# Kernel tuning notes

Hardware: AMD Instinct MI355X
Metric: run time of the kernel (lower is better)

Reference implementation:

```python
import jax, jax.numpy as jnp
import numpy as np

G, N, F_IN = 1024, 256, 128
HID = [256, 256, 256]
KS = [32, 16, 8]
N_OUT = 2


def _graph_conv(adj, x, W, b, act):
    # DGL GraphConv, norm='both': h = D^{-1/2} A D^{-1/2} X W + b
    deg = adj.sum(-1)                                   # [G, n]
    norm = jax.lax.rsqrt(jnp.maximum(deg, 1.0))[..., None]
    h = (x * norm) @ W                                  # [G, n, d_out]
    h = jnp.einsum('gnm,gmd->gnd', adj, h) * norm + b
    return act(h) if act is not None else h


def _sag_pool(adj, x, Ws, bs, k):
    # SAGPool: score via GraphConv, keep top-k nodes, gate by tanh(score),
    # take induced subgraph adjacency.
    score = _graph_conv(adj, x, Ws, bs, None)[..., 0]   # [G, n]
    sv, idx = jax.lax.top_k(score, k)                   # [G, k]
    x_sel = jnp.take_along_axis(x, idx[:, :, None], axis=1) * jnp.tanh(sv)[:, :, None]
    a = jnp.take_along_axis(adj, idx[:, :, None], axis=1)
    a = jnp.take_along_axis(a, idx[:, None, :], axis=2)  # [G, k, k]
    return a, x_sel


def _sum_max_readout(x):
    return jnp.concatenate([x.sum(axis=1), x.max(axis=1)], axis=-1)  # [G, 2d]


def setup_inputs() -> dict:
    key = jax.random.key(0)
    ks = jax.random.split(key, 16)
    feat = jax.random.normal(ks[0], (G, N, F_IN), dtype=jnp.float32)
    # sparse-ish symmetric binary adjacency, avg degree ~ 16
    a = (jax.random.uniform(ks[1], (G, N, N)) < (16.0 / N)).astype(jnp.float32)
    adj = jnp.maximum(a, jnp.swapaxes(a, 1, 2))

    def glorot(k, shp):
        lim = float(np.sqrt(6.0 / (shp[0] + shp[1])))
        return jax.random.uniform(k, shp, jnp.float32, -lim, lim)

    dims = [F_IN] + HID
    inp = {'feat': feat, 'adj': adj}
    for i in range(3):
        inp[f'W{i}'] = glorot(ks[2 + i], (dims[i], dims[i + 1]))
        inp[f'b{i}'] = jnp.zeros((dims[i + 1],), jnp.float32)
        inp[f'Ws{i}'] = glorot(ks[5 + i], (dims[i + 1], 1))
        inp[f'bs{i}'] = jnp.zeros((1,), jnp.float32)
    inp['Wd1'] = glorot(ks[8], (2 * sum(HID), 128))
    inp['bd1'] = jnp.zeros((128,), jnp.float32)
    inp['Wd2'] = glorot(ks[9], (128, N_OUT))
    inp['bd2'] = jnp.zeros((N_OUT,), jnp.float32)
    return inp


def reference(feat, adj, W0, b0, Ws0, bs0, W1, b1, Ws1, bs1, W2, b2, Ws2, bs2,
              Wd1, bd1, Wd2, bd2):
    act = jax.nn.leaky_relu  # F.leaky_relu, slope 0.01
    Wgs = [(W0, b0), (W1, b1), (W2, b2)]
    Wss = [(Ws0, bs0), (Ws1, bs1), (Ws2, bs2)]
    readouts = []
    x, a = feat, adj
    for i in range(3):
        x = _graph_conv(a, x, Wgs[i][0], Wgs[i][1], act)
        a, x = _sag_pool(a, x, Wss[i][0], Wss[i][1], KS[i])
        readouts.append(_sum_max_readout(x))
    merged = jnp.concatenate(readouts, axis=1)          # [G, 2*sum(HID)]
    # dropout omitted (deterministic eval reference)
    h = act(merged @ Wd1 + bd1)
    out = jax.nn.sigmoid(h @ Wd2 + bd2)                 # [G, n_output]
    return out
```

## Files before the change

### kernel.cpp

```cpp
#include <hip/hip_runtime.h>
#include <math.h>

constexpr int GG  = 1024;
constexpr int NN  = 256;
constexpr int FF  = 128;
constexpr int DD  = 256;
constexpr int KS0 = 32, KS1 = 16, KS2 = 8;

__device__ __forceinline__ float lrelu(float x){ return x >= 0.f ? x : 0.01f*x; }

__device__ __forceinline__ unsigned short f2bf(float f) {
  unsigned u = __float_as_uint(f);
  unsigned r = (u + 0x7FFFu + ((u >> 16) & 1u)) >> 16;
  return (unsigned short)r;
}
__device__ __forceinline__ float bf2f(unsigned short h) {
  return __uint_as_float(((unsigned)h) << 16);
}

typedef __attribute__((ext_vector_type(8)))  __bf16 bf16x8;
typedef __attribute__((ext_vector_type(16))) float  f32x16;

union Frag8 { unsigned short us[8]; unsigned long long u64[2]; bf16x8 v; };

typedef __attribute__((address_space(1))) void gvoid;
typedef __attribute__((address_space(3))) void lvoid;
__device__ __forceinline__ void async_cp16(const unsigned short* g, unsigned short* l) {
  __builtin_amdgcn_global_load_lds((const gvoid*)g, (lvoid*)l, 16, 0, 0);
}

__global__ void k_splitW_all(const float* __restrict__ Wa, const float* __restrict__ Wb,
                             const float* __restrict__ Wc,
                             unsigned short* __restrict__ oa, unsigned short* __restrict__ ob,
                             unsigned short* __restrict__ oc) {
  int e = blockIdx.x*256 + threadIdx.x;
  if (e >= FF*DD + 2*DD*DD) return;
  const float* W; unsigned short* out; int K;
  if (e < FF*DD)                { W = Wa; out = oa; K = FF; }
  else if (e < FF*DD + DD*DD)   { e -= FF*DD; W = Wb; out = ob; K = DD; }
  else                          { e -= FF*DD + DD*DD; W = Wc; out = oc; K = DD; }
  int j    = e & 7;
  int lane = (e >> 3) & 63;
  int nt   = (e >> 9) & 7;
  int s    = (e >> 12) & 1;
  int kti  = e >> 13;
  int n = nt*32 + (lane & 31);
  int k = kti*32 + s*16 + ((lane >> 5) << 3) + j;
  float x = W[(size_t)k*DD + n];
  unsigned short h1 = f2bf(x);  float r1 = x - bf2f(h1);
  unsigned short h2 = f2bf(r1); float r2 = r1 - bf2f(h2);
  unsigned short h3 = f2bf(r2);
  out[e] = h1; out[DD*K + e] = h2; out[2*DD*K + e] = h3;
}

__global__ void k_maskrow(const float* __restrict__ adj, float* __restrict__ norm0,
                          unsigned long long* __restrict__ mask) {
  int row = blockIdx.x*4 + (threadIdx.x >> 6);
  int lane = threadIdx.x & 63;
  const float* ar = adj + (size_t)row*NN;
  float f0 = ar[lane], f1 = ar[64 + lane], f2 = ar[128 + lane], f3 = ar[192 + lane];
  unsigned long long m0 = __ballot(f0 > 0.5f);
  unsigned long long m1 = __ballot(f1 > 0.5f);
  unsigned long long m2 = __ballot(f2 > 0.5f);
  unsigned long long m3 = __ballot(f3 > 0.5f);
  if (lane < 4) {
    unsigned long long mm = lane == 0 ? m0 : lane == 1 ? m1 : lane == 2 ? m2 : m3;
    mask[(size_t)row*4 + lane] = mm;
  }
  if (lane == 0) {
    int cnt = __popcll(m0) + __popcll(m1) + __popcll(m2) + __popcll(m3);
    norm0[row] = rsqrtf(fmaxf((float)cnt, 1.0f));
  }
}

__global__ __launch_bounds__(256, 4) void k_spmm_s(
    const float* __restrict__ feat, const unsigned long long* __restrict__ mask,
    const float* __restrict__ norm0, float* __restrict__ T0) {
  constexpr int ST = 36;
  __shared__ float ls[NN*ST];
  __shared__ float snorm[NN];
  int bid = blockIdx.x;
  int g = bid >> 2, q = bid & 3;
  int t = threadIdx.x;
  const float* Xg = feat + (size_t)g*NN*FF + q*32;

  snorm[t] = norm0[g*NN + t];
  const unsigned long long* mp = mask + ((size_t)g*NN + t)*4;
  unsigned long long mrow[4];
  #pragma unroll
  for (int w = 0; w < 4; ++w) mrow[w] = mp[w];
  __syncthreads();

  #pragma unroll
  for (int i = 0; i < 8; ++i) {
    int e = t + i*256;
    int r = e >> 3, c4 = (e & 7)*4;
    float4 v = *reinterpret_cast<const float4*>(Xg + (size_t)r*FF + c4);
    float nv = snorm[r];
    v.x *= nv; v.y *= nv; v.z *= nv; v.w *= nv;
    *reinterpret_cast<float4*>(&ls[r*ST + c4]) = v;
  }
  __syncthreads();

  float4 acc[8];
  #pragma unroll
  for (int i = 0; i < 8; ++i) acc[i] = make_float4(0.f, 0.f, 0.f, 0.f);
  #pragma unroll
  for (int w = 0; w < 4; ++w) {
    unsigned long long m = mrow[w];
    while (m) {
      int c = __builtin_ctzll(m);
      const float4* xp = reinterpret_cast<const float4*>(&ls[(w*64 + c)*ST]);
      #pragma unroll
      for (int i = 0; i < 8; ++i) {
        float4 v = xp[i];
        acc[i].x += v.x; acc[i].y += v.y; acc[i].z += v.z; acc[i].w += v.w;
      }
      m &= m - 1;
    }
  }
  float* op = T0 + ((size_t)g*NN + t)*FF + q*32;
  #pragma unroll
  for (int i = 0; i < 8; ++i)
    *reinterpret_cast<float4*>(op + i*4) = acc[i];
}

__global__ __launch_bounds__(256, 2) void k_gemm0(
    const float* __restrict__ Tmat, const unsigned short* __restrict__ Wk,
    const float* __restrict__ normv, const float* __restrict__ bias,
    const float* __restrict__ Ws, float* __restrict__ hs) {
  __shared__ unsigned short bsh[3*8192];
  int t = threadIdx.x;
  int lane = t & 63, wave = t >> 6;
  int lm = lane & 31, lh = lane >> 5;
  int rowbase = blockIdx.x*128 + wave*32;

  f32x16 acc[8];
  #pragma unroll
  for (int nt = 0; nt < 8; ++nt) acc[nt] = (f32x16)0.0f;

  for (int kti = 0; kti < 4; ++kti) {
    int kt = kti*32;
    float4 af[2][2];
    #pragma unroll
    for (int s = 0; s < 2; ++s) {
      const float* ap = Tmat + (size_t)(rowbase + lm)*FF + kt + s*16 + lh*8;
      af[s][0] = *reinterpret_cast<const float4*>(ap);
      af[s][1] = *reinterpret_cast<const float4*>(ap + 4);
    }
    __syncthreads();
    #pragma unroll
    for (int sp = 0; sp < 3; ++sp)
      #pragma unroll
      for (int r = 0; r < 4; ++r) {
        const unsigned short* src = Wk + (size_t)sp*DD*FF + (size_t)kti*8192 + r*2048 + t*8;
        unsigned short* dst = bsh + sp*8192 + r*2048 + t*8;
        async_cp16(src, dst);
      }
    __syncthreads();
    Frag8 afr[2][3];
    #pragma unroll
    for (int s = 0; s < 2; ++s) {
      const float* fv = &af[s][0].x;
      #pragma unroll
      for (int j = 0; j < 8; ++j) {
        float x = fv[j];
        unsigned short h1 = f2bf(x);  float r1 = x - bf2f(h1);
        unsigned short h2 = f2bf(r1); float r2 = r1 - bf2f(h2);
        afr[s][0].us[j] = h1; afr[s][1].us[j] = h2; afr[s][2].us[j] = f2bf(r2);
      }
    }
    #pragma unroll
    for (int s = 0; s < 2; ++s)
      #pragma unroll
      for (int nt = 0; nt < 8; ++nt) {
        const unsigned short* bp = bsh + ((s*8 + nt)*64 + lane)*8;
        Frag8 b0_, b1_, b2_;
        b0_.v = *reinterpret_cast<const bf16x8*>(bp);
        b1_.v = *reinterpret_cast<const bf16x8*>(bp + 8192);
        b2_.v = *reinterpret_cast<const bf16x8*>(bp + 16384);
        acc[nt] = __builtin_amdgcn_mfma_f32_32x32x16_bf16(afr[s][0].v, b0_.v, acc[nt], 0,0,0);
        acc[nt] = __builtin_amdgcn_mfma_f32_32x32x16_bf16(afr[s][0].v, b1_.v, acc[nt], 0,0,0);
        acc[nt] = __builtin_amdgcn_mfma_f32_32x32x16_bf16(afr[s][1].v, b0_.v, acc[nt], 0,0,0);
        acc[nt] = __builtin_amdgcn_mfma_f32_32x32x16_bf16(afr[s][0].v, b2_.v, acc[nt], 0,0,0);
        acc[nt] = __builtin_amdgcn_mfma_f32_32x32x16_bf16(afr[s][2].v, b0_.v, acc[nt], 0,0,0);
        acc[nt] = __builtin_amdgcn_mfma_f32_32x32x16_bf16(afr[s][1].v, b1_.v, acc[nt], 0,0,0);
      }
  }

  float bcol[8], wcol[8];
  #pragma unroll
  for (int nt = 0; nt < 8; ++nt) { int col = nt*32 + lm; bcol[nt] = bias[col]; wcol[nt] = Ws[col]; }
  float hsum[16];
  #pragma unroll
  for (int r = 0; r < 16; ++r) {
    int row = rowbase + (r & 3) + 8*(r >> 2) + 4*lh;
    float nv = normv[row];
    float hp = 0.f;
    #pragma unroll
    for (int nt = 0; nt < 8; ++nt) hp += lrelu(nv*acc[nt][r] + bcol[nt])*wcol[nt];
    hsum[r] = hp;
  }
  #pragma unroll
  for (int off = 1; off <= 16; off <<= 1)
    #pragma unroll
    for (int r = 0; r < 16; ++r) hsum[r] += __shfl_xor(hsum[r], off);
  if (lm == 0)
    #pragma unroll
    for (int r = 0; r < 16; ++r) {
      int row = rowbase + (r & 3) + 8*(r >> 2) + 4*lh;
      hs[row] = normv[row]*hsum[r];
    }
}

__global__ __launch_bounds__(256) void k_topk_sel0(
    const unsigned long long* __restrict__ mask, const float* __restrict__ hs,
    const float* __restrict__ norm0, const float* __restrict__ bs,
    const float* __restrict__ T0, const float* __restrict__ W0,
    const float* __restrict__ b0, float* __restrict__ x_sel,
    float* __restrict__ a1, float* __restrict__ merged) {
  __shared__ float sh[NN];
  __shared__ float ssc[NN];
  __shared__ float sT[KS0*FF];
  __shared__ int sidx[KS0]; __shared__ float stv[KS0]; __shared__ float snv[KS0];
  int g = blockIdx.x, t = threadIdx.x;

  sh[t] = hs[g*NN + t];
  __syncthreads();
  const unsigned long long* mr = mask + ((size_t)g*NN + t)*4;
  float s = 0.f;
  #pragma unroll
  for (int w = 0; w < 4; ++w) {
    unsigned long long m = mr[w];
    const float* base = sh + w*64;
    while (m) {
      int c = __builtin_ctzll(m);
      s += base[c];
      m &= m - 1;
    }
  }
  ssc[t] = norm0[g*NN + t]*s + bs[0];
  __syncthreads();
  if (t < 64) {
    float sv[4]; int si[4];
    #pragma unroll
    for (int e = 0; e < 4; ++e) { sv[e] = ssc[e*64 + t]; si[e] = e*64 + t; }
    for (int kk = 0; kk < KS0; ++kk) {
      float bs_ = -INFINITY; int bi = 1 << 30;
      #pragma unroll
      for (int e = 0; e < 4; ++e)
        if (sv[e] > bs_ || (sv[e] == bs_ && si[e] < bi)) { bs_ = sv[e]; bi = si[e]; }
      for (int off = 32; off; off >>= 1) {
        float os = __shfl_xor(bs_, off);
        int oi = __shfl_xor(bi, off);
        if (os > bs_ || (os == bs_ && oi < bi)) { bs_ = os; bi = oi; }
      }
      if (t == 0) { sidx[kk] = bi; stv[kk] = tanhf(bs_); }
      #pragma unroll
      for (int e = 0; e < 4; ++e) if (si[e] == bi) sv[e] = -INFINITY;
    }
  }
  __syncthreads();
  if (t < KS0) snv[t] = norm0[g*NN + sidx[t]];
  #pragma unroll
  for (int i = 0; i < 4; ++i) {
    int e4 = t + i*256;
    int r = e4 >> 5, c4 = e4 & 31;
    reinterpret_cast<float4*>(sT)[e4] =
        *reinterpret_cast<const float4*>(&T0[((size_t)g*NN + sidx[r])*FF + c4*4]);
  }
  __syncthreads();
  float sum[KS0];
  #pragma unroll
  for (int j = 0; j < KS0; ++j) sum[j] = 0.f;
  for (int k = 0; k < FF; k += 4) {
    float4 w;
    w.x = W0[(size_t)(k+0)*DD + t]; w.y = W0[(size_t)(k+1)*DD + t];
    w.z = W0[(size_t)(k+2)*DD + t]; w.w = W0[(size_t)(k+3)*DD + t];
    #pragma unroll
    for (int j = 0; j < KS0; ++j) {
      float4 tv4 = *reinterpret_cast<const float4*>(&sT[j*FF + k]);
      sum[j] += tv4.x*w.x + tv4.y*w.y + tv4.z*w.z + tv4.w*w.w;
    }
  }
  float b = b0[t];
  float ssum = 0.f, mx = -INFINITY;
  #pragma unroll
  for (int j = 0; j < KS0; ++j) {
    float val = lrelu(snv[j]*sum[j] + b) * stv[j];
    x_sel[((size_t)g*KS0 + j)*DD + t] = val;
    ssum += val; mx = fmaxf(mx, val);
  }
  merged[(size_t)g*1536 + t] = ssum;
  merged[(size_t)g*1536 + 256 + t] = mx;
  for (int e = t; e < KS0*KS0; e += 256) {
    int r = e >> 5, c = e & 31;
    int nr = sidx[r], nc = sidx[c];
    unsigned long long m = mask[((size_t)g*NN + nr)*4 + (nc >> 6)];
    a1[(size_t)g*KS0*KS0 + e] = (float)((m >> (nc & 63)) & 1ull);
  }
}

__global__ __launch_bounds__(256, 2) void k_fused1(
    const float* __restrict__ a, const float* __restrict__ xin,
    const unsigned short* __restrict__ Wk, const float* __restrict__ bias,
    const float* __restrict__ Ws, const float* __restrict__ bs,
    float* __restrict__ x_sel_out, float* __restrict__ a_out,
    float* __restrict__ merged) {
  constexpr int n = KS0;
  constexpr int kp = KS1;
  constexpr int TP = DD + 4;
  __shared__ float sa[n*n];
  __shared__ float bufA[n*DD];
  __shared__ float sT[n*TP];
  __shared__ float snorm[n]; __shared__ float shs[n]; __shared__ float ssc[n];
  __shared__ int sidx[kp]; __shared__ float stv[kp];
  int g = blockIdx.x, t = threadIdx.x;
  int lane = t & 63, wave = t >> 6, lm = lane & 31, lh = lane >> 5;

  for (int e = t; e < n*n; e += 256) sa[e] = a[(size_t)g*n*n + e];
  __syncthreads();
  if (t < n) {
    float dg = 0.f;
    for (int m = 0; m < n; ++m) dg += sa[m*n + t];
    snorm[t] = rsqrtf(fmaxf(dg, 1.f));
  }
  __syncthreads();
  {
    const float4* xp = reinterpret_cast<const float4*>(xin + (size_t)g*n*DD);
    #pragma unroll
    for (int i = 0; i < (n*DD/4)/256; ++i) {
      int e4 = t + i*256;
      float4 v = xp[e4];
      float nv = snorm[e4 >> 6];
      v.x *= nv; v.y *= nv; v.z *= nv; v.w *= nv;
      reinterpret_cast<float4*>(bufA)[e4] = v;
    }
  }
  __syncthreads();
  {
    float acc2[n];
    #pragma unroll
    for (int r = 0; r < n; ++r) acc2[r] = 0.f;
    for (int m = 0; m < n; ++m) {
      float xv = bufA[m*DD + t];
      #pragma unroll
      for (int r = 0; r < n; ++r) acc2[r] += sa[r*n + m]*xv;
    }
    #pragma unroll
    for (int r = 0; r < n; ++r) sT[r*TP + t] = acc2[r];
  }
  __syncthreads();

  f32x16 acc[2];
  acc[0] = (f32x16)0.0f; acc[1] = (f32x16)0.0f;
  for (int kti = 0; kti < DD/32; ++kti) {
    int kt = kti*32;
    Frag8 afr[2][3];
    #pragma unroll
    for (int s = 0; s < 2; ++s) {
      float4 af4[2];
      const float* ap = &sT[lm*TP + kt + s*16 + lh*8];
      af4[0] = *reinterpret_cast<const float4*>(ap);
      af4[1] = *reinterpret_cast<const float4*>(ap + 4);
      const float* fv = &af4[0].x;
      #pragma unroll
      for (int j = 0; j < 8; ++j) {
        float x = fv[j];
        unsigned short h1 = f2bf(x);  float r1 = x - bf2f(h1);
        unsigned short h2 = f2bf(r1); float r2 = r1 - bf2f(h2);
        afr[s][0].us[j] = h1; afr[s][1].us[j] = h2; afr[s][2].us[j] = f2bf(r2);
      }
    }
    #pragma unroll
    for (int s = 0; s < 2; ++s)
      #pragma unroll
      for (int ntl = 0; ntl < 2; ++ntl) {
        int ct = wave*2 + ntl;
        size_t boff = ((((size_t)kti*2 + s)*8 + ct)*64 + lane)*8;
        Frag8 b0_, b1_, b2_;
        b0_.v = *reinterpret_cast<const bf16x8*>(Wk + boff);
        b1_.v = *reinterpret_cast<const bf16x8*>(Wk + (size_t)DD*DD + boff);
        b2_.v = *reinterpret_cast<const bf16x8*>(Wk + (size_t)2*DD*DD + boff);
        acc[ntl] = __builtin_amdgcn_mfma_f32_32x32x16_bf16(afr[s][0].v, b0_.v, acc[ntl], 0,0,0);
        acc[ntl] = __builtin_amdgcn_mfma_f32_32x32x16_bf16(afr[s][0].v, b1_.v, acc[ntl], 0,0,0);
        acc[ntl] = __builtin_amdgcn_mfma_f32_32x32x16_bf16(afr[s][1].v, b0_.v, acc[ntl], 0,0,0);
        acc[ntl] = __builtin_amdgcn_mfma_f32_32x32x16_bf16(afr[s][0].v, b2_.v, acc[ntl], 0,0,0);
        acc[ntl] = __builtin_amdgcn_mfma_f32_32x32x16_bf16(afr[s][2].v, b0_.v, acc[ntl], 0,0,0);
        acc[ntl] = __builtin_amdgcn_mfma_f32_32x32x16_bf16(afr[s][1].v, b1_.v, acc[ntl], 0,0,0);
      }
  }

  #pragma unroll
  for (int ntl = 0; ntl < 2; ++ntl) {
    int colbase = wave*64 + ntl*32 + lm;
    float bc = bias[colbase];
    #pragma unroll
    for (int r = 0; r < 16; ++r) {
      int row = (r & 3) + 8*(r >> 2) + 4*lh;
      bufA[row*DD + colbase] = lrelu(snorm[row]*acc[ntl][r] + bc);
    }
  }
  __syncthreads();
  if (wave == 0) {
    float wcol[8];
    #pragma unroll
    for (int nt = 0; nt < 8; ++nt) wcol[nt] = Ws[nt*32 + lm];
    float hsum[16];
    #pragma unroll
    for (int r = 0; r < 16; ++r) {
      int row = (r & 3) + 8*(r >> 2) + 4*lh;
      float hp = 0.f;
      #pragma unroll
      for (int nt = 0; nt < 8; ++nt) hp += bufA[row*DD + nt*32 + lm]*wcol[nt];
      hsum[r] = hp;
    }
    #pragma unroll
    for (int off = 1; off <= 16; off <<= 1)
      #pragma unroll
      for (int r = 0; r < 16; ++r) hsum[r] += __shfl_xor(hsum[r], off);
    if (lm == 0)
      #pragma unroll
      for (int r = 0; r < 16; ++r) {
        int row = (r & 3) + 8*(r >> 2) + 4*lh;
        shs[row] = snorm[row]*hsum[r];
      }
  }
  __syncthreads();
  if (t < n) {
    float s = 0.f;
    for (int m = 0; m < n; ++m) s += sa[m*n + t]*shs[m];
    ssc[t] = snorm[t]*s + bs[0];
  }
  __syncthreads();
  if (t < 64) {
    float sc = (t < n) ? ssc[t] : -INFINITY;
    int si = (t < n) ? t : (1 << 30);
    for (int kk = 0; kk < kp; ++kk) {
      float bs_ = sc; int bi = si;
      for (int off = 32; off; off >>= 1) {
        float os = __shfl_xor(bs_, off);
        int oi = __shfl_xor(bi, off);
        if (os > bs_ || (os == bs_ && oi < bi)) { bs_ = os; bi = oi; }
      }
      if (t == 0) { sidx[kk] = bi; stv[kk] = tanhf(bs_); }
      if (si == bi) sc = -INFINITY;
    }
  }
  __syncthreads();
  float sum = 0.f, mx = -INFINITY;
  #pragma unroll
  for (int j = 0; j < kp; ++j) {
    float v = bufA[sidx[j]*DD + t] * stv[j];
    x_sel_out[((size_t)g*kp + j)*DD + t] = v;
    sum += v; mx = fmaxf(mx, v);
  }
  merged[(size_t)g*1536 + 512 + t] = sum;
  merged[(size_t)g*1536 + 768 + t] = mx;
  { int r = t >> 4, c = t & 15;
    a_out[(size_t)g*kp*kp + t] = sa[sidx[r]*n + sidx[c]]; }
}

__global__ __launch_bounds__(256, 2) void k_fused2(
    const float* __restrict__ a, const float* __restrict__ xin,
    const unsigned short* __restrict__ Wk, const float* __restrict__ bias,
    const float* __restrict__ Ws, const float* __restrict__ bs,
    float* __restrict__ merged) {
  constexpr int n = KS1;
  constexpr int kp = KS2;
  constexpr int TP = DD + 4;
  __shared__ float sa[n*n];
  __shared__ float bufA[n*DD];
  __shared__ float sT[n*TP];
  __shared__ float snorm[n]; __shared__ float shs[n]; __shared__ float ssc[n];
  __shared__ int sidx[kp]; __shared__ float stv[kp];
  int g = blockIdx.x, t = threadIdx.x;
  int lane = t & 63, wave = t >> 6, lm = lane & 31, lh = lane >> 5;

  for (int e = t; e < n*n; e += 256) sa[e] = a[(size_t)g*n*n + e];
  __syncthreads();
  if (t < n) {
    float dg = 0.f;
    for (int m = 0; m < n; ++m) dg += sa[m*n + t];
    snorm[t] = rsqrtf(fmaxf(dg, 1.f));
  }
  __syncthreads();
  {
    const float4* xp = reinterpret_cast<const float4*>(xin + (size_t)g*n*DD);
    #pragma unroll
    for (int i = 0; i < (n*DD/4)/256; ++i) {
      int e4 = t + i*256;
      float4 v = xp[e4];
      float nv = snorm[e4 >> 6];
      v.x *= nv; v.y *= nv; v.z *= nv; v.w *= nv;
      reinterpret_cast<float4*>(bufA)[e4] = v;
    }
  }
  __syncthreads();
  {
    float acc2[n];
    #pragma unroll
    for (int r = 0; r < n; ++r) acc2[r] = 0.f;
    for (int m = 0; m < n; ++m) {
      float xv = bufA[m*DD + t];
      #pragma unroll
      for (int r = 0; r < n; ++r) acc2[r] += sa[r*n + m]*xv;
    }
    #pragma unroll
    for (int r = 0; r < n; ++r) sT[r*TP + t] = acc2[r];
  }
  __syncthreads();

  f32x16 acc[2];
  acc[0] = (f32x16)0.0f; acc[1] = (f32x16)0.0f;
  for (int kti = 0; kti < DD/32; ++kti) {
    int kt = kti*32;
    Frag8 afr[2][3];
    #pragma unroll
    for (int s = 0; s < 2; ++s) {
      float4 af4[2];
      if (lm < n) {
        const float* ap = &sT[lm*TP + kt + s*16 + lh*8];
        af4[0] = *reinterpret_cast<const float4*>(ap);
        af4[1] = *reinterpret_cast<const float4*>(ap + 4);
      } else {
        af4[0] = make_float4(0.f, 0.f, 0.f, 0.f);
        af4[1] = make_float4(0.f, 0.f, 0.f, 0.f);
      }
      const float* fv = &af4[0].x;
      #pragma unroll
      for (int j = 0; j < 8; ++j) {
        float x = fv[j];
        unsigned short h1 = f2bf(x);  float r1 = x - bf2f(h1);
        unsigned short h2 = f2bf(r1); float r2 = r1 - bf2f(h2);
        afr[s][0].us[j] = h1; afr[s][1].us[j] = h2; afr[s][2].us[j] = f2bf(r2);
      }
    }
    #pragma unroll
    for (int s = 0; s < 2; ++s)
      #pragma unroll
      for (int ntl = 0; ntl < 2; ++ntl) {
        int ct = wave*2 + ntl;
        size_t boff = ((((size_t)kti*2 + s)*8 + ct)*64 + lane)*8;
        Frag8 b0_, b1_, b2_;
        b0_.v = *reinterpret_cast<const bf16x8*>(Wk + boff);
        b1_.v = *reinterpret_cast<const bf16x8*>(Wk + (size_t)DD*DD + boff);
        b2_.v = *reinterpret_cast<const bf16x8*>(Wk + (size_t)2*DD*DD + boff);
        acc[ntl] = __builtin_amdgcn_mfma_f32_32x32x16_bf16(afr[s][0].v, b0_.v, acc[ntl], 0,0,0);
        acc[ntl] = __builtin_amdgcn_mfma_f32_32x32x16_bf16(afr[s][0].v, b1_.v, acc[ntl], 0,0,0);
        acc[ntl] = __builtin_amdgcn_mfma_f32_32x32x16_bf16(afr[s][1].v, b0_.v, acc[ntl], 0,0,0);
        acc[ntl] = __builtin_amdgcn_mfma_f32_32x32x16_bf16(afr[s][0].v, b2_.v, acc[ntl], 0,0,0);
        acc[ntl] = __builtin_amdgcn_mfma_f32_32x32x16_bf16(afr[s][2].v, b0_.v, acc[ntl], 0,0,0);
        acc[ntl] = __builtin_amdgcn_mfma_f32_32x32x16_bf16(afr[s][1].v, b1_.v, acc[ntl], 0,0,0);
      }
  }

  #pragma unroll
  for (int ntl = 0; ntl < 2; ++ntl) {
    int colbase = wave*64 + ntl*32 + lm;
    float bc = bias[colbase];
    #pragma unroll
    for (int r = 0; r < 16; ++r) {
      int row = (r & 3) + 8*(r >> 2) + 4*lh;
      if (row < n) bufA[row*DD + colbase] = lrelu(snorm[row]*acc[ntl][r] + bc);
    }
  }
  __syncthreads();
  if (wave == 0) {
    float wcol[8];
    #pragma unroll
    for (int nt = 0; nt < 8; ++nt) wcol[nt] = Ws[nt*32 + lm];
    float hsum[16];
    #pragma unroll
    for (int r = 0; r < 16; ++r) {
      int row = (r & 3) + 8*(r >> 2) + 4*lh;
      float hp = 0.f;
      if (row < n) {
        #pragma unroll
        for (int nt = 0; nt < 8; ++nt) hp += bufA[row*DD + nt*32 + lm]*wcol[nt];
      }
      hsum[r] = hp;
    }
    #pragma unroll
    for (int off = 1; off <= 16; off <<= 1)
      #pragma unroll
      for (int r = 0; r < 16; ++r) hsum[r] += __shfl_xor(hsum[r], off);
    if (lm == 0)
      #pragma unroll
      for (int r = 0; r < 16; ++r) {
        int row = (r & 3) + 8*(r >> 2) + 4*lh;
        if (row < n) shs[row] = snorm[row]*hsum[r];
      }
  }
  __syncthreads();
  if (t < n) {
    float s = 0.f;
    for (int m = 0; m < n; ++m) s += sa[m*n + t]*shs[m];
    ssc[t] = snorm[t]*s + bs[0];
  }
  __syncthreads();
  if (t < 64) {
    float sc = (t < n) ? ssc[t] : -INFINITY;
    int si = (t < n) ? t : (1 << 30);
    for (int kk = 0; kk < kp; ++kk) {
      float bs_ = sc; int bi = si;
      for (int off = 32; off; off >>= 1) {
        float os = __shfl_xor(bs_, off);
        int oi = __shfl_xor(bi, off);
        if (os > bs_ || (os == bs_ && oi < bi)) { bs_ = os; bi = oi; }
      }
      if (t == 0) { sidx[kk] = bi; stv[kk] = tanhf(bs_); }
      if (si == bi) sc = -INFINITY;
    }
  }
  __syncthreads();
  float sum = 0.f, mx = -INFINITY;
  #pragma unroll
  for (int j = 0; j < kp; ++j) {
    float v = bufA[sidx[j]*DD + t] * stv[j];
    sum += v; mx = fmaxf(mx, v);
  }
  merged[(size_t)g*1536 + 1024 + t] = sum;
  merged[(size_t)g*1536 + 1280 + t] = mx;
}

__global__ void k_mlp(const float* __restrict__ merged, const float* __restrict__ Wd1,
                      const float* __restrict__ bd1, const float* __restrict__ Wd2,
                      const float* __restrict__ bd2, float* __restrict__ out) {
  __shared__ float sm[4*1536];
  __shared__ float sh[4][128];
  int g0 = blockIdx.x*4; int t = threadIdx.x;
  for (int i = t; i < 4*1536; i += 128) sm[i] = merged[(size_t)g0*1536 + i];
  __syncthreads();
  float a0 = 0.f, a1 = 0.f, a2 = 0.f, a3 = 0.f;
  for (int kk = 0; kk < 1536; ++kk) {
    float w = Wd1[(size_t)kk*128 + t];
    a0 += sm[kk]*w; a1 += sm[1536 + kk]*w; a2 += sm[3072 + kk]*w; a3 += sm[4608 + kk]*w;
  }
  float b = bd1[t];
  sh[0][t] = lrelu(a0 + b); sh[1][t] = lrelu(a1 + b);
  sh[2][t] = lrelu(a2 + b); sh[3][t] = lrelu(a3 + b);
  __syncthreads();
  if (t < 8) {
    int gi = t >> 1, c = t & 1;
    float o = 0.f;
    for (int kk = 0; kk < 128; ++kk) o += sh[gi][kk]*Wd2[kk*2 + c];
    out[(size_t)(g0 + gi)*2 + c] = 1.f/(1.f + expf(-(o + bd2[c])));
  }
}

extern "C" void kernel_launch(void* const* d_in, const int* in_sizes, int n_in,
                              void* d_out, int out_size, void* d_ws, size_t ws_size,
                              hipStream_t stream) {
  const float* feat = (const float*)d_in[0];
  const float* adj  = (const float*)d_in[1];
  const float* W0 = (const float*)d_in[2];  const float* b0  = (const float*)d_in[3];
  const float* Ws0= (const float*)d_in[4];  const float* bs0 = (const float*)d_in[5];
  const float* W1 = (const float*)d_in[6];  const float* b1  = (const float*)d_in[7];
  const float* Ws1= (const float*)d_in[8];  const float* bs1 = (const float*)d_in[9];
  const float* W2 = (const float*)d_in[10]; const float* b2  = (const float*)d_in[11];
  const float* Ws2= (const float*)d_in[12]; const float* bs2 = (const float*)d_in[13];
  const float* Wd1= (const float*)d_in[14]; const float* bd1 = (const float*)d_in[15];
  const float* Wd2= (const float*)d_in[16]; const float* bd2 = (const float*)d_in[17];
  float* out = (float*)d_out;

  char* ws = (char*)d_ws;
  size_t off = 0;
  auto alloc = [&](size_t bytes) -> char* {
    char* p = ws + off; off += (bytes + 255) & ~(size_t)255; return p;
  };
  float* norm0 = (float*)alloc((size_t)GG*NN*4);
  unsigned long long* mask0 = (unsigned long long*)alloc((size_t)GG*NN*4*8);
  float* hs0   = (float*)alloc((size_t)GG*NN*4);
  float* merged= (float*)alloc((size_t)GG*1536*4);
  unsigned short* W0s = (unsigned short*)alloc((size_t)3*FF*DD*2);
  unsigned short* W1s = (unsigned short*)alloc((size_t)3*DD*DD*2);
  unsigned short* W2s = (unsigned short*)alloc((size_t)3*DD*DD*2);
  float* T0     = (float*)alloc((size_t)GG*NN*FF*4);
  float* x_sel1 = (float*)alloc((size_t)GG*KS0*DD*4);
  float* a1     = (float*)alloc((size_t)GG*KS0*KS0*4);
  float* x_sel2 = (float*)alloc((size_t)GG*KS1*DD*4);
  float* a2     = (float*)alloc((size_t)GG*KS1*KS1*4);

  k_splitW_all<<<(FF*DD + 2*DD*DD)/256, 256, 0, stream>>>(W0, W1, W2, W0s, W1s, W2s);

  k_maskrow<<<GG*NN/4, 256, 0, stream>>>(adj, norm0, mask0);
  k_spmm_s<<<4*GG, 256, 0, stream>>>(feat, mask0, norm0, T0);
  k_gemm0<<<GG*NN/128, 256, 0, stream>>>(T0, W0s, norm0, b0, Ws0, hs0);
  k_topk_sel0<<<GG, 256, 0, stream>>>(mask0, hs0, norm0, bs0, T0, W0, b0, x_sel1, a1, merged);

  k_fused1<<<GG, 256, 0, stream>>>(a1, x_sel1, W1s, b1, Ws1, bs1, x_sel2, a2, merged);

  k_fused2<<<GG, 256, 0, stream>>>(a2, x_sel2, W2s, b2, Ws2, bs2, merged);

  k_mlp<<<GG/4, 128, 0, stream>>>(merged, Wd1, bd1, Wd2, bd2, out);

  (void)in_sizes; (void)n_in; (void)out_size; (void)ws_size;
}
```

Before: 915.5 us.

## Fuse layer-0 GEMM score computation with top-k selection into one per-graph kernel

```diff
diff --git a/kernel.cpp b/kernel.cpp
--- a/kernel.cpp
+++ b/kernel.cpp
@@ -125,15 +125,23 @@
     *reinterpret_cast<float4*>(op + i*4) = acc[i];
 }
 
-__global__ __launch_bounds__(256, 2) void k_gemm0(
+__global__ __launch_bounds__(512, 2) void k_gemm_topk0(
     const float* __restrict__ Tmat, const unsigned short* __restrict__ Wk,
     const float* __restrict__ normv, const float* __restrict__ bias,
-    const float* __restrict__ Ws, float* __restrict__ hs) {
+    const float* __restrict__ Ws, const unsigned long long* __restrict__ mask,
+    const float* __restrict__ bs, const float* __restrict__ W0,
+    const float* __restrict__ b0, float* __restrict__ x_sel,
+    float* __restrict__ a1, float* __restrict__ merged) {
   __shared__ unsigned short bsh[3*8192];
+  __shared__ float shs[NN];
+  __shared__ float ssc[NN];
+  __shared__ int sidx[KS0]; __shared__ float stv[KS0]; __shared__ float snv[KS0];
+  int g = blockIdx.x;
   int t = threadIdx.x;
   int lane = t & 63, wave = t >> 6;
   int lm = lane & 31, lh = lane >> 5;
-  int rowbase = blockIdx.x*128 + wave*32;
+  int rowbase = wave*32;
+  const size_t growbase = (size_t)g*NN;
 
   f32x16 acc[8];
   #pragma unroll
@@ -144,19 +152,18 @@
     float4 af[2][2];
     #pragma unroll
     for (int s = 0; s < 2; ++s) {
-      const float* ap = Tmat + (size_t)(rowbase + lm)*FF + kt + s*16 + lh*8;
+      const float* ap = Tmat + (growbase + rowbase + lm)*FF + kt + s*16 + lh*8;
       af[s][0] = *reinterpret_cast<const float4*>(ap);
       af[s][1] = *reinterpret_cast<const float4*>(ap + 4);
     }
     __syncthreads();
     #pragma unroll
-    for (int sp = 0; sp < 3; ++sp)
-      #pragma unroll
-      for (int r = 0; r < 4; ++r) {
-        const unsigned short* src = Wk + (size_t)sp*DD*FF + (size_t)kti*8192 + r*2048 + t*8;
-        unsigned short* dst = bsh + sp*8192 + r*2048 + t*8;
-        async_cp16(src, dst);
-      }
+    for (int rr = 0; rr < 6; ++rr) {
+      int sp = rr >> 1, half = rr & 1;
+      const unsigned short* src = Wk + (size_t)sp*DD*FF + (size_t)kti*8192 + half*4096 + t*8;
+      unsigned short* dst = bsh + sp*8192 + half*4096 + t*8;
+      async_cp16(src, dst);
+    }
     __syncthreads();
     Frag8 afr[2][3];
     #pragma unroll
@@ -188,58 +195,48 @@
       }
   }
 
-  float bcol[8], wcol[8];
-  #pragma unroll
-  for (int nt = 0; nt < 8; ++nt) { int col = nt*32 + lm; bcol[nt] = bias[col]; wcol[nt] = Ws[col]; }
-  float hsum[16];
-  #pragma unroll
-  for (int r = 0; r < 16; ++r) {
-    int row = rowbase + (r & 3) + 8*(r >> 2) + 4*lh;
-    float nv = normv[row];
-    float hp = 0.f;
-    #pragma unroll
-    for (int nt = 0; nt < 8; ++nt) hp += lrelu(nv*acc[nt][r] + bcol[nt])*wcol[nt];
-    hsum[r] = hp;
-  }
-  #pragma unroll
-  for (int off = 1; off <= 16; off <<= 1)
-    #pragma unroll
-    for (int r = 0; r < 16; ++r) hsum[r] += __shfl_xor(hsum[r], off);
-  if (lm == 0)
+  {
+    float bcol[8], wcol[8];
+    #pragma unroll
+    for (int nt = 0; nt < 8; ++nt) { int col = nt*32 + lm; bcol[nt] = bias[col]; wcol[nt] = Ws[col]; }
+    float hsum[16];
     #pragma unroll
     for (int r = 0; r < 16; ++r) {
       int row = rowbase + (r & 3) + 8*(r >> 2) + 4*lh;
-      hs[row] = normv[row]*hsum[r];
-    }
-}
-
-__global__ __launch_bounds__(256) void k_topk_sel0(
-    const unsigned long long* __restrict__ mask, const float* __restrict__ hs,
-    const float* __restrict__ norm0, const float* __restrict__ bs,
-    const float* __restrict__ T0, const float* __restrict__ W0,
-    const float* __restrict__ b0, float* __restrict__ x_sel,
-    float* __restrict__ a1, float* __restrict__ merged) {
-  __shared__ float sh[NN];
-  __shared__ float ssc[NN];
-  __shared__ float sT[KS0*FF];
-  __shared__ int sidx[KS0]; __shared__ float stv[KS0]; __shared__ float snv[KS0];
-  int g = blockIdx.x, t = threadIdx.x;
-
-  sh[t] = hs[g*NN + t];
-  __syncthreads();
-  const unsigned long long* mr = mask + ((size_t)g*NN + t)*4;
-  float s = 0.f;
-  #pragma unroll
-  for (int w = 0; w < 4; ++w) {
-    unsigned long long m = mr[w];
-    const float* base = sh + w*64;
-    while (m) {
-      int c = __builtin_ctzll(m);
-      s += base[c];
-      m &= m - 1;
-    }
-  }
-  ssc[t] = norm0[g*NN + t]*s + bs[0];
+      float nv = normv[growbase + row];
+      float hp = 0.f;
+      #pragma unroll
+      for (int nt = 0; nt < 8; ++nt) hp += lrelu(nv*acc[nt][r] + bcol[nt])*wcol[nt];
+      hsum[r] = hp;
+    }
+    #pragma unroll
+    for (int off = 1; off <= 16; off <<= 1)
+      #pragma unroll
+      for (int r = 0; r < 16; ++r) hsum[r] += __shfl_xor(hsum[r], off);
+    if (lm == 0)
+      #pragma unroll
+      for (int r = 0; r < 16; ++r) {
+        int row = rowbase + (r & 3) + 8*(r >> 2) + 4*lh;
+        shs[row] = normv[growbase + row]*hsum[r];
+      }
+  }
+  __syncthreads();
+
+  if (t < NN) {
+    const unsigned long long* mr = mask + (growbase + t)*4;
+    float s = 0.f;
+    #pragma unroll
+    for (int w = 0; w < 4; ++w) {
+      unsigned long long m = mr[w];
+      const float* base = shs + w*64;
+      while (m) {
+        int c = __builtin_ctzll(m);
+        s += base[c];
+        m &= m - 1;
+      }
+    }
+    ssc[t] = normv[growbase + t]*s + bs[0];
+  }
   __syncthreads();
   if (t < 64) {
     float sv[4]; int si[4];
@@ -261,42 +258,46 @@
     }
   }
   __syncthreads();
-  if (t < KS0) snv[t] = norm0[g*NN + sidx[t]];
-  #pragma unroll
-  for (int i = 0; i < 4; ++i) {
-    int e4 = t + i*256;
+
+  float* sT = reinterpret_cast<float*>(bsh);
+  if (t < KS0) snv[t] = normv[growbase + sidx[t]];
+  #pragma unroll
+  for (int i = 0; i < 2; ++i) {
+    int e4 = t + i*512;
     int r = e4 >> 5, c4 = e4 & 31;
     reinterpret_cast<float4*>(sT)[e4] =
-        *reinterpret_cast<const float4*>(&T0[((size_t)g*NN + sidx[r])*FF + c4*4]);
-  }
-  __syncthreads();
-  float sum[KS0];
-  #pragma unroll
-  for (int j = 0; j < KS0; ++j) sum[j] = 0.f;
-  for (int k = 0; k < FF; k += 4) {
-    float4 w;
-    w.x = W0[(size_t)(k+0)*DD + t]; w.y = W0[(size_t)(k+1)*DD + t];
-    w.z = W0[(size_t)(k+2)*DD + t]; w.w = W0[(size_t)(k+3)*DD + t];
+        *reinterpret_cast<const float4*>(&Tmat[(growbase + sidx[r])*FF + c4*4]);
+  }
+  __syncthreads();
+  if (t < DD) {
+    float sum[KS0];
+    #pragma unroll
+    for (int j = 0; j < KS0; ++j) sum[j] = 0.f;
+    for (int k = 0; k < FF; k += 4) {
+      float4 w;
+      w.x = W0[(size_t)(k+0)*DD + t]; w.y = W0[(size_t)(k+1)*DD + t];
+      w.z = W0[(size_t)(k+2)*DD + t]; w.w = W0[(size_t)(k+3)*DD + t];
+      #pragma unroll
+      for (int j = 0; j < KS0; ++j) {
+        float4 tv4 = *reinterpret_cast<const float4*>(&sT[j*FF + k]);
+        sum[j] += tv4.x*w.x + tv4.y*w.y + tv4.z*w.z + tv4.w*w.w;
+      }
+    }
+    float b = b0[t];
+    float ssum = 0.f, mx = -INFINITY;
     #pragma unroll
     for (int j = 0; j < KS0; ++j) {
-      float4 tv4 = *reinterpret_cast<const float4*>(&sT[j*FF + k]);
-      sum[j] += tv4.x*w.x + tv4.y*w.y + tv4.z*w.z + tv4.w*w.w;
-    }
-  }
-  float b = b0[t];
-  float ssum = 0.f, mx = -INFINITY;
-  #pragma unroll
-  for (int j = 0; j < KS0; ++j) {
-    float val = lrelu(snv[j]*sum[j] + b) * stv[j];
-    x_sel[((size_t)g*KS0 + j)*DD + t] = val;
-    ssum += val; mx = fmaxf(mx, val);
-  }
-  merged[(size_t)g*1536 + t] = ssum;
-  merged[(size_t)g*1536 + 256 + t] = mx;
-  for (int e = t; e < KS0*KS0; e += 256) {
+      float val = lrelu(snv[j]*sum[j] + b) * stv[j];
+      x_sel[((size_t)g*KS0 + j)*DD + t] = val;
+      ssum += val; mx = fmaxf(mx, val);
+    }
+    merged[(size_t)g*1536 + t] = ssum;
+    merged[(size_t)g*1536 + 256 + t] = mx;
+  }
+  for (int e = t; e < KS0*KS0; e += 512) {
     int r = e >> 5, c = e & 31;
     int nr = sidx[r], nc = sidx[c];
-    unsigned long long m = mask[((size_t)g*NN + nr)*4 + (nc >> 6)];
+    unsigned long long m = mask[(growbase + nr)*4 + (nc >> 6)];
     a1[(size_t)g*KS0*KS0 + e] = (float)((m >> (nc & 63)) & 1ull);
   }
 }
@@ -671,7 +672,6 @@
   };
   float* norm0 = (float*)alloc((size_t)GG*NN*4);
   unsigned long long* mask0 = (unsigned long long*)alloc((size_t)GG*NN*4*8);
-  float* hs0   = (float*)alloc((size_t)GG*NN*4);
   float* merged= (float*)alloc((size_t)GG*1536*4);
   unsigned short* W0s = (unsigned short*)alloc((size_t)3*FF*DD*2);
   unsigned short* W1s = (unsigned short*)alloc((size_t)3*DD*DD*2);
@@ -686,8 +686,8 @@
 
   k_maskrow<<<GG*NN/4, 256, 0, stream>>>(adj, norm0, mask0);
   k_spmm_s<<<4*GG, 256, 0, stream>>>(feat, mask0, norm0, T0);
-  k_gemm0<<<GG*NN/128, 256, 0, stream>>>(T0, W0s, norm0, b0, Ws0, hs0);
-  k_topk_sel0<<<GG, 256, 0, stream>>>(mask0, hs0, norm0, bs0, T0, W0, b0, x_sel1, a1, merged);
+  k_gemm_topk0<<<GG, 512, 0, stream>>>(T0, W0s, norm0, b0, Ws0, mask0, bs0, W0, b0,
+                                       x_sel1, a1, merged);
 
   k_fused1<<<GG, 256, 0, stream>>>(a1, x_sel1, W1s, b1, Ws1, bs1, x_sel2, a2, merged);
 
```

Result: slower. 1.028 ms (+12.3%).
